# Optimization experiments

Measured on AMD Instinct MI355X. Metric: run time of the kernel, lower is better.

Reference implementation:

```python
import jax, jax.numpy as jnp
import numpy as np

DIM = 32
DN = ('NCDHW', 'OIDHW', 'NCDHW')


def _dwconv(x, w, b, pad, dil):
    # depthwise 3D conv, x: [N, C, D, H, W], w: [C, 1, kd, kh, kw]
    y = jax.lax.conv_general_dilated(
        x, w, window_strides=(1, 1, 1),
        padding=[(pad[0], pad[0]), (pad[1], pad[1]), (pad[2], pad[2])],
        rhs_dilation=dil, dimension_numbers=DN,
        feature_group_count=x.shape[1])
    return y + b[None, :, None, None, None]


def setup_inputs() -> dict:
    key = jax.random.key(0)
    ks = jax.random.split(key, 11)
    B, T, C, D, H, W = 1, 8, DIM, 32, 64, 64
    x = jax.random.normal(ks[0], (B, T, C, D, H, W), dtype=jnp.float32)
    s = 0.1
    w0z = jax.random.normal(ks[1], (C, 1, 3, 1, 1), dtype=jnp.float32) * s
    b0z = jax.random.normal(ks[2], (C,), dtype=jnp.float32) * s
    w0x = jax.random.normal(ks[3], (C, 1, 1, 3, 1), dtype=jnp.float32) * s
    b0x = jax.random.normal(ks[4], (C,), dtype=jnp.float32) * s
    w0y = jax.random.normal(ks[5], (C, 1, 1, 1, 3), dtype=jnp.float32) * s
    b0y = jax.random.normal(ks[6], (C,), dtype=jnp.float32) * s
    wsz = jax.random.normal(ks[7], (C, 1, 5, 1, 1), dtype=jnp.float32) * s
    bsz = jax.random.normal(ks[8], (C,), dtype=jnp.float32) * s
    wp = jax.random.normal(ks[9], (C, C, 1, 1, 1), dtype=jnp.float32) * s
    bp = jax.random.normal(ks[10], (C,), dtype=jnp.float32) * s
    return {"x": x, "w0z": w0z, "b0z": b0z, "w0x": w0x, "b0x": b0x,
            "w0y": w0y, "b0y": b0y, "wsz": wsz, "bsz": bsz,
            "wp": wp, "bp": bp}


def reference(x, w0z, b0z, w0x, b0x, w0y, b0y, wsz, bsz, wp, bp):
    B, T, C, D, H, W = x.shape
    h = x.reshape(B * T, C, D, H, W)  # TimeDistributed flatten
    res = h
    h = _dwconv(h, w0z, b0z, (1, 0, 0), (1, 1, 1))
    h = _dwconv(h, w0x, b0x, (0, 1, 0), (1, 1, 1))
    h = _dwconv(h, w0y, b0y, (0, 0, 1), (1, 1, 1))
    # forward applies conv_spatial_z three times (faithful to source)
    for _ in range(3):
        h = _dwconv(h, wsz, bsz, (4, 0, 0), (2, 1, 1))
    # pointwise 1x1x1 conv (full channel mixing)
    h = jax.lax.conv_general_dilated(
        h, wp, window_strides=(1, 1, 1),
        padding=[(0, 0)] * 3, dimension_numbers=DN)
    h = h + bp[None, :, None, None, None]
    out = res * h
    return out.reshape(B, T, C, D, H, W)
```

## Files before the change

kernel.cpp:

```cpp
#include <hip/hip_runtime.h>

constexpr int NT = 8;
constexpr int C  = 32;
constexpr int D  = 32;
constexpr int H  = 64;
constexpr int W  = 64;
constexpr int ROWS = 4;
constexpr int SP = D * H * W;
constexpr int HW = H * W;

__global__ __launch_bounds__(256, 3)
void dw_chain(const float* __restrict__ x,
              const float* __restrict__ w0z, const float* __restrict__ b0z,
              const float* __restrict__ w0x, const float* __restrict__ b0x,
              const float* __restrict__ w0y, const float* __restrict__ b0y,
              const float* __restrict__ wsz, const float* __restrict__ bsz,
              float* __restrict__ hdw)
{
    const int rr  = blockIdx.x;
    const int lid = (rr & 7) * (NT * C * (H / ROWS) / 8) + (rr >> 3);
    const int htile = lid % (H / ROWS);
    const int c     = (lid / (H / ROWS)) % C;
    const int n     = lid / ((H / ROWS) * C);

    const int tid = threadIdx.x;
    const int w   = tid & 63;
    const int hg  = htile * ROWS + (tid >> 6);

    const float* xc = x + ((size_t)n * C + c) * SP;

    const float wz0 = w0z[c*3+0], wz1 = w0z[c*3+1], wz2 = w0z[c*3+2];
    const float wx1 = w0x[c*3+1];
    const float wy0 = w0y[c*3+0], wy1 = w0y[c*3+1], wy2 = w0y[c*3+2];
    const float bz = b0z[c], bx = b0x[c], by = b0y[c], bs = bsz[c];
    float wsk[5];
    #pragma unroll
    for (int k = 0; k < 5; ++k) wsk[k] = wsz[c*5+k];

    const float wxk0 = (hg > 0)     ? w0x[c*3+0] : 0.f;
    const float wxk2 = (hg < H - 1) ? w0x[c*3+2] : 0.f;
    const int   hm = (hg > 0)     ? hg - 1 : 0;
    const int   hp = (hg < H - 1) ? hg + 1 : H - 1;

    const float* p0 = xc + (size_t)hm * W + w;
    const float* p1 = xc + (size_t)hg * W + w;
    const float* p2 = xc + (size_t)hp * W + w;
    float a0[D], a1[D], a2[D];
    #pragma unroll
    for (int d = 0; d < D; ++d) {
        a0[d] = p0[(size_t)d * HW];
        a1[d] = p1[(size_t)d * HW];
        a2[d] = p2[(size_t)d * HW];
    }
    __builtin_amdgcn_sched_barrier(0);

    float hrow[D];
    #pragma unroll
    for (int d = 0; d < D; ++d)
        hrow[d] = wxk0 * a0[d] + wx1 * a1[d] + wxk2 * a2[d];

    const float cb = bx + (wxk0 + wx1 + wxk2) * bz;
    float acc2[D];
    #pragma unroll
    for (int d = 0; d < D; ++d) {
        float t = cb + wz1 * hrow[d];
        if (d > 0)     t += wz0 * hrow[d - 1];
        if (d < D - 1) t += wz2 * hrow[d + 1];
        acc2[d] = t;
    }

    const bool has_l = (w > 0), has_r = (w < W - 1);
    float acc3[D];
    #pragma unroll
    for (int d = 0; d < D; ++d) {
        float left  = __shfl_up(acc2[d], 1);
        float right = __shfl_down(acc2[d], 1);
        float t = by + wy1 * acc2[d];
        if (has_l) t += wy0 * left;
        if (has_r) t += wy2 * right;
        acc3[d] = t;
    }

    #pragma unroll
    for (int it = 0; it < 3; ++it) {
        float s[D];
        #pragma unroll
        for (int d = 0; d < D; ++d) {
            float t = bs;
            #pragma unroll
            for (int k = 0; k < 5; ++k) {
                int j = d + 2 * k - 4;
                if (j >= 0 && j < D) t += wsk[k] * acc3[j];
            }
            s[d] = t;
        }
        #pragma unroll
        for (int d = 0; d < D; ++d) acc3[d] = s[d];
    }

    float* oc = hdw + ((size_t)n * C + c) * SP + (size_t)hg * W + w;
    #pragma unroll
    for (int d = 0; d < D; ++d) oc[(size_t)d * HW] = acc3[d];
}

__global__ __launch_bounds__(256)
void pw_mul(const float* __restrict__ x,
            const float* __restrict__ wp, const float* __restrict__ bp,
            float* __restrict__ io)
{
    const size_t p = (size_t)blockIdx.x * 256 + threadIdx.x;
    const size_t n  = p / SP;
    const size_t sp = p % SP;
    const size_t base = n * (size_t)C * SP + sp;

    float v[C];
    #pragma unroll
    for (int ci = 0; ci < C; ++ci) v[ci] = io[base + (size_t)ci * SP];

    for (int co = 0; co < C; ++co) {
        float y = bp[co];
        #pragma unroll
        for (int ci = 0; ci < C; ++ci) y += wp[co * C + ci] * v[ci];
        const size_t idx = base + (size_t)co * SP;
        io[idx] = x[idx] * y;
    }
}

extern "C" void kernel_launch(void* const* d_in, const int* in_sizes, int n_in,
                              void* d_out, int out_size, void* d_ws, size_t ws_size,
                              hipStream_t stream)
{
    const float* x   = (const float*)d_in[0];
    const float* w0z = (const float*)d_in[1];
    const float* b0z = (const float*)d_in[2];
    const float* w0x = (const float*)d_in[3];
    const float* b0x = (const float*)d_in[4];
    const float* w0y = (const float*)d_in[5];
    const float* b0y = (const float*)d_in[6];
    const float* wsz = (const float*)d_in[7];
    const float* bsz = (const float*)d_in[8];
    const float* wp  = (const float*)d_in[9];
    const float* bp  = (const float*)d_in[10];
    float* out = (float*)d_out;

    const int gridA = NT * C * (H / ROWS);
    dw_chain<<<gridA, 256, 0, stream>>>(x, w0z, b0z, w0x, b0x, w0y, b0y,
                                        wsz, bsz, out);

    const int positions = NT * SP;
    pw_mul<<<positions / 256, 256, 0, stream>>>(x, wp, bp, out);
}
```

Baseline: 114.0 us.

## Fuse depthwise chain and pointwise mix into one kernel per (n, h) row

```diff
diff --git a/kernel.cpp b/kernel.cpp
--- a/kernel.cpp
+++ b/kernel.cpp
@@ -5,124 +5,122 @@
 constexpr int D  = 32;
 constexpr int H  = 64;
 constexpr int W  = 64;
-constexpr int ROWS = 4;
 constexpr int SP = D * H * W;
 constexpr int HW = H * W;
 
-__global__ __launch_bounds__(256, 3)
-void dw_chain(const float* __restrict__ x,
-              const float* __restrict__ w0z, const float* __restrict__ b0z,
-              const float* __restrict__ w0x, const float* __restrict__ b0x,
-              const float* __restrict__ w0y, const float* __restrict__ b0y,
-              const float* __restrict__ wsz, const float* __restrict__ bsz,
-              float* __restrict__ hdw)
+__global__ __launch_bounds__(512, 6)
+void lska_fused(const float* __restrict__ x,
+                const float* __restrict__ w0z, const float* __restrict__ b0z,
+                const float* __restrict__ w0x, const float* __restrict__ b0x,
+                const float* __restrict__ w0y, const float* __restrict__ b0y,
+                const float* __restrict__ wsz, const float* __restrict__ bsz,
+                const float* __restrict__ wp,  const float* __restrict__ bp,
+                float* __restrict__ out)
 {
     const int rr  = blockIdx.x;
-    const int lid = (rr & 7) * (NT * C * (H / ROWS) / 8) + (rr >> 3);
-    const int htile = lid % (H / ROWS);
-    const int c     = (lid / (H / ROWS)) % C;
-    const int n     = lid / ((H / ROWS) * C);
+    const int lid = (rr & 7) * (NT * H / 8) + (rr >> 3);
+    const int n   = lid >> 6;
+    const int hg  = lid & 63;
 
     const int tid = threadIdx.x;
     const int w   = tid & 63;
-    const int hg  = htile * ROWS + (tid >> 6);
+    const int r   = tid >> 6;
 
-    const float* xc = x + ((size_t)n * C + c) * SP;
+    #pragma unroll 1
+    for (int cc = 0; cc < 4; ++cc) {
+        const int c = r + cc * 8;
+        const float* xc = x + ((size_t)n * C + c) * SP;
 
-    const float wz0 = w0z[c*3+0], wz1 = w0z[c*3+1], wz2 = w0z[c*3+2];
-    const float wx1 = w0x[c*3+1];
-    const float wy0 = w0y[c*3+0], wy1 = w0y[c*3+1], wy2 = w0y[c*3+2];
-    const float bz = b0z[c], bx = b0x[c], by = b0y[c], bs = bsz[c];
-    float wsk[5];
-    #pragma unroll
-    for (int k = 0; k < 5; ++k) wsk[k] = wsz[c*5+k];
+        const float wz0 = w0z[c*3+0], wz1 = w0z[c*3+1], wz2 = w0z[c*3+2];
+        const float wx1 = w0x[c*3+1];
+        const float wy0 = w0y[c*3+0], wy1 = w0y[c*3+1], wy2 = w0y[c*3+2];
+        const float bz = b0z[c], bx = b0x[c], by = b0y[c], bs = bsz[c];
+        float wsk[5];
+        #pragma unroll
+        for (int k = 0; k < 5; ++k) wsk[k] = wsz[c*5+k];
 
-    const float wxk0 = (hg > 0)     ? w0x[c*3+0] : 0.f;
-    const float wxk2 = (hg < H - 1) ? w0x[c*3+2] : 0.f;
-    const int   hm = (hg > 0)     ? hg - 1 : 0;
-    const int   hp = (hg < H - 1) ? hg + 1 : H - 1;
+        const float wxk0 = (hg > 0)     ? w0x[c*3+0] : 0.f;
+        const float wxk2 = (hg < H - 1) ? w0x[c*3+2] : 0.f;
+        const int   hm = (hg > 0)     ? hg - 1 : 0;
+        const int   hp = (hg < H - 1) ? hg + 1 : H - 1;
 
-    const float* p0 = xc + (size_t)hm * W + w;
-    const float* p1 = xc + (size_t)hg * W + w;
-    const float* p2 = xc + (size_t)hp * W + w;
-    float a0[D], a1[D], a2[D];
-    #pragma unroll
-    for (int d = 0; d < D; ++d) {
-        a0[d] = p0[(size_t)d * HW];
-        a1[d] = p1[(size_t)d * HW];
-        a2[d] = p2[(size_t)d * HW];
-    }
-    __builtin_amdgcn_sched_barrier(0);
+        const float* p0 = xc + (size_t)hm * W + w;
+        const float* p1 = xc + (size_t)hg * W + w;
+        const float* p2 = xc + (size_t)hp * W + w;
 
-    float hrow[D];
-    #pragma unroll
-    for (int d = 0; d < D; ++d)
-        hrow[d] = wxk0 * a0[d] + wx1 * a1[d] + wxk2 * a2[d];
+        float hrow[D];
+        #pragma unroll
+        for (int d = 0; d < D; ++d) {
+            float a0 = p0[(size_t)d * HW];
+            float a1 = p1[(size_t)d * HW];
+            float a2 = p2[(size_t)d * HW];
+            hrow[d] = wxk0 * a0 + wx1 * a1 + wxk2 * a2;
+        }
 
-    const float cb = bx + (wxk0 + wx1 + wxk2) * bz;
-    float acc2[D];
-    #pragma unroll
-    for (int d = 0; d < D; ++d) {
-        float t = cb + wz1 * hrow[d];
-        if (d > 0)     t += wz0 * hrow[d - 1];
-        if (d < D - 1) t += wz2 * hrow[d + 1];
-        acc2[d] = t;
+        const float cb = bx + (wxk0 + wx1 + wxk2) * bz;
+        float acc2[D];
+        #pragma unroll
+        for (int d = 0; d < D; ++d) {
+            float t = cb + wz1 * hrow[d];
+            if (d > 0)     t += wz0 * hrow[d - 1];
+            if (d < D - 1) t += wz2 * hrow[d + 1];
+            acc2[d] = t;
+        }
+
+        const bool has_l = (w > 0), has_r = (w < W - 1);
+        float acc3[D];
+        #pragma unroll
+        for (int d = 0; d < D; ++d) {
+            float left  = __shfl_up(acc2[d], 1);
+            float right = __shfl_down(acc2[d], 1);
+            float t = by + wy1 * acc2[d];
+            if (has_l) t += wy0 * left;
+            if (has_r) t += wy2 * right;
+            acc3[d] = t;
+        }
+
+        #pragma unroll
+        for (int it = 0; it < 3; ++it) {
+            float s[D];
+            #pragma unroll
+            for (int d = 0; d < D; ++d) {
+                float t = bs;
+                #pragma unroll
+                for (int k = 0; k < 5; ++k) {
+                    int j = d + 2 * k - 4;
+                    if (j >= 0 && j < D) t += wsk[k] * acc3[j];
+                }
+                s[d] = t;
+            }
+            #pragma unroll
+            for (int d = 0; d < D; ++d) acc3[d] = s[d];
+        }
+
+        float* oc = out + ((size_t)n * C + c) * SP + (size_t)hg * W + w;
+        #pragma unroll
+        for (int d = 0; d < D; ++d) oc[(size_t)d * HW] = acc3[d];
     }
 
-    const bool has_l = (w > 0), has_r = (w < W - 1);
-    float acc3[D];
-    #pragma unroll
-    for (int d = 0; d < D; ++d) {
-        float left  = __shfl_up(acc2[d], 1);
-        float right = __shfl_down(acc2[d], 1);
-        float t = by + wy1 * acc2[d];
-        if (has_l) t += wy0 * left;
-        if (has_r) t += wy2 * right;
-        acc3[d] = t;
-    }
+    __syncthreads();
 
-    #pragma unroll
-    for (int it = 0; it < 3; ++it) {
-        float s[D];
+    const int dq = tid >> 6;
+    #pragma unroll 1
+    for (int k = 0; k < 4; ++k) {
+        const int d = dq + k * 8;
+        const size_t base = (size_t)n * C * SP + (size_t)d * HW
+                          + (size_t)hg * W + w;
+
+        float v[C];
         #pragma unroll
-        for (int d = 0; d < D; ++d) {
-            float t = bs;
+        for (int ci = 0; ci < C; ++ci) v[ci] = out[base + (size_t)ci * SP];
+
+        for (int co = 0; co < C; ++co) {
+            float y = bp[co];
             #pragma unroll
-            for (int k = 0; k < 5; ++k) {
-                int j = d + 2 * k - 4;
-                if (j >= 0 && j < D) t += wsk[k] * acc3[j];
-            }
-            s[d] = t;
+            for (int ci = 0; ci < C; ++ci) y += wp[co * C + ci] * v[ci];
+            const size_t idx = base + (size_t)co * SP;
+            out[idx] = x[idx] * y;
         }
-        #pragma unroll
-        for (int d = 0; d < D; ++d) acc3[d] = s[d];
-    }
-
-    float* oc = hdw + ((size_t)n * C + c) * SP + (size_t)hg * W + w;
-    #pragma unroll
-    for (int d = 0; d < D; ++d) oc[(size_t)d * HW] = acc3[d];
-}
-
-__global__ __launch_bounds__(256)
-void pw_mul(const float* __restrict__ x,
-            const float* __restrict__ wp, const float* __restrict__ bp,
-            float* __restrict__ io)
-{
-    const size_t p = (size_t)blockIdx.x * 256 + threadIdx.x;
-    const size_t n  = p / SP;
-    const size_t sp = p % SP;
-    const size_t base = n * (size_t)C * SP + sp;
-
-    float v[C];
-    #pragma unroll
-    for (int ci = 0; ci < C; ++ci) v[ci] = io[base + (size_t)ci * SP];
-
-    for (int co = 0; co < C; ++co) {
-        float y = bp[co];
-        #pragma unroll
-        for (int ci = 0; ci < C; ++ci) y += wp[co * C + ci] * v[ci];
-        const size_t idx = base + (size_t)co * SP;
-        io[idx] = x[idx] * y;
     }
 }
 
@@ -143,10 +141,7 @@
     const float* bp  = (const float*)d_in[10];
     float* out = (float*)d_out;
 
-    const int gridA = NT * C * (H / ROWS);
-    dw_chain<<<gridA, 256, 0, stream>>>(x, w0z, b0z, w0x, b0x, w0y, b0y,
-                                        wsz, bsz, out);
-
-    const int positions = NT * SP;
-    pw_mul<<<positions / 256, 256, 0, stream>>>(x, wp, bp, out);
+    const int grid = NT * H;
+    lska_fused<<<grid, 512, 0, stream>>>(
+        x, w0z, b0z, w0x, b0x, w0y, b0y, wsz, bsz, wp, bp, out);
 }
```

Result: slower. 170.6 us (+49.6%).
